# Performance work log

Hardware: AMD Instinct MI355X
Metric: run time of the kernel (lower is better)

The kernel has to match this reference:

```python
import jax, jax.numpy as jnp
import numpy as np

N = 8192          # total neurons (n)
IN_NEURONS = 1024 # input_neurons
OUT_NEURONS = 256 # output_neurons


def setup_inputs() -> dict:
    key = jax.random.key(0)
    k1, k2 = jax.random.split(key)
    x = jax.random.normal(k1, (1, IN_NEURONS), dtype=jnp.float32)
    # learned adjacency weight (original uses kaiming_uniform; scale kept small for stability)
    W = jax.random.normal(k2, (N, N), dtype=jnp.float32) * 0.01
    return {"x": x, "W": W, "num_steps": 4}


def reference(x, W, num_steps):
    n = W.shape[0]
    # load_input_neurons: state = (W.T * pad(x[0], n)).T  ==  W * s0[:, None]
    s0 = jnp.pad(x[0], (0, n - x.shape[1]))        # [n]
    state = W * s0[:, None]                        # [n, n]

    # step(): next = sum_i(W.T * state[i]) then .T  ==  W * colsum(state)[:, None]
    def body(state, _):
        col_sum = state.sum(axis=0)                # [n]
        return W * col_sum[:, None], None

    state, _ = jax.lax.scan(body, state, None, length=num_steps)

    # extract_output_neurons: diagonal entries state[-i, -i], i = OUT..1
    return jnp.diagonal(state)[-OUT_NEURONS:]      # [OUT_NEURONS]
```

## Files before the change

### kernel.cpp

```cpp
#include <hip/hip_runtime.h>


namespace {
constexpr int N = 8192;
constexpr int NF4 = N / 4;
constexpr int IN_N = 1024;
constexpr int OUT_N = 256;
constexpr int BT = 256;

constexpr int NCT = 8;
constexpr int R1R = 32;
constexpr int R2R = 128;
constexpr int SL1 = IN_N / R1R;
constexpr int SL2 = N / R2R;

constexpr size_t OFF_V1 = 0;
constexpr size_t OFF_V2 = 8192;
constexpr size_t OFF_V3 = 16384;
constexpr size_t OFF_V4 = 24576;
constexpr size_t OFF_P  = 32768;

typedef float f4 __attribute__((ext_vector_type(4)));
}

__global__ void zero_vecs(float* __restrict__ ws) {
  int i = blockIdx.x * blockDim.x + threadIdx.x;
  if (i < 3 * N + OUT_N) ws[i] = 0.0f;
}

template <int ROWS>
__global__ __launch_bounds__(BT) void gemv_slab(const float* __restrict__ W,
                                                const float* __restrict__ vin,
                                                float* __restrict__ P) {
  __shared__ float sv[ROWS];
  const int b = blockIdx.x, t = threadIdx.x;
  const int ct = b & (NCT - 1);
  const int rs = b >> 3;
  const int i0 = rs * ROWS;
  for (int i = t; i < ROWS; i += BT) sv[i] = vin[i0 + i];
  __syncthreads();
  const f4* __restrict__ W4 = reinterpret_cast<const f4*>(W);
  const int cf = ct * BT + t;
  f4 acc = (f4)(0.f);
#pragma unroll 8
  for (int i = 0; i < ROWS; ++i) {
    const f4 w = __builtin_nontemporal_load(W4 + (size_t)(i0 + i) * NF4 + cf);
    acc += w * sv[i];
  }
  reinterpret_cast<f4*>(P)[(size_t)rs * NF4 + cf] = acc;
}

template <int CS>
__global__ __launch_bounds__(BT) void reduce_cols(const float* __restrict__ P,
                                                  float* __restrict__ v) {
  const int j = blockIdx.x * BT + threadIdx.x;
  const int c0 = blockIdx.y * CS;
  float a = 0.f;
#pragma unroll
  for (int c = 0; c < CS; ++c) a += P[(size_t)(c0 + c) * N + j];
  atomicAdd(v + j, a);
}

__global__ __launch_bounds__(64) void gemv_tail(const float* __restrict__ W,
                                                const float* __restrict__ v3,
                                                float* __restrict__ v4) {
  __shared__ float sv[32];
  const int b = blockIdx.x, t = threadIdx.x;
  const int i0 = b * 32;
  if (t < 32) sv[t] = v3[i0 + t];
  __syncthreads();
  const f4* __restrict__ W4 = reinterpret_cast<const f4*>(W);
  f4 a = (f4)(0.f);
#pragma unroll 4
  for (int i = 0; i < 32; ++i) {
    const f4 w = W4[(size_t)(i0 + i) * NF4 + 1984 + t];
    a += w * sv[i];
  }
  atomicAdd(v4 + 4 * t + 0, a.x);
  atomicAdd(v4 + 4 * t + 1, a.y);
  atomicAdd(v4 + 4 * t + 2, a.z);
  atomicAdd(v4 + 4 * t + 3, a.w);
}

__global__ void diag_scale(const float* __restrict__ W,
                           const float* __restrict__ v4,
                           float* __restrict__ out) {
  const int t = threadIdx.x;
  const size_t j = (size_t)(N - OUT_N + t);
  out[t] = W[j * (N + 1)] * v4[t];
}

extern "C" void kernel_launch(void* const* d_in, const int* in_sizes, int n_in,
                              void* d_out, int out_size, void* d_ws, size_t ws_size,
                              hipStream_t stream) {
  const float* x = (const float*)d_in[0];
  const float* W = (const float*)d_in[1];
  float* ws = (float*)d_ws;
  float* v1 = ws + OFF_V1;
  float* v2 = ws + OFF_V2;
  float* v3 = ws + OFF_V3;
  float* v4 = ws + OFF_V4;
  float* P  = ws + OFF_P;
  float* out = (float*)d_out;

  zero_vecs<<<(3 * N + OUT_N + 255) / 256, 256, 0, stream>>>(ws);

  gemv_slab<R1R><<<SL1 * NCT, BT, 0, stream>>>(W, x, P);
  reduce_cols<16><<<dim3(N / BT, SL1 / 16), BT, 0, stream>>>(P, v1);

  gemv_slab<R2R><<<SL2 * NCT, BT, 0, stream>>>(W, v1, P);
  reduce_cols<16><<<dim3(N / BT, SL2 / 16), BT, 0, stream>>>(P, v2);

  gemv_slab<R2R><<<SL2 * NCT, BT, 0, stream>>>(W, v2, P);
  reduce_cols<16><<<dim3(N / BT, SL2 / 16), BT, 0, stream>>>(P, v3);

  gemv_tail<<<N / 32, 64, 0, stream>>>(W, v3, v4);

  diag_scale<<<1, OUT_N, 0, stream>>>(W, v4, out);
}
```

Measured before the change: 435.4 us.

## Fuse partial-sum reduction into GEMV via atomics and fold diagonal scale into tail

The GEMV slab kernels now accumulate their per-slab partial column sums straight into the output vector with float atomics, so the partial buffer P and the separate reduce_cols kernels go away. The tail kernel also multiplies by the diagonal entries and atomically adds into the output, which removes the diag_scale launch. The output is zeroed in the initial kernel, and the tail's W reads become nontemporal. This removes several launches and the P write/read round trip, in exchange for many more atomic operations (64 slabs per column) and nondeterministic summation order.

```diff
diff --git a/kernel.cpp b/kernel.cpp
--- a/kernel.cpp
+++ b/kernel.cpp
@@ -17,21 +17,20 @@
 constexpr size_t OFF_V1 = 0;
 constexpr size_t OFF_V2 = 8192;
 constexpr size_t OFF_V3 = 16384;
-constexpr size_t OFF_V4 = 24576;
-constexpr size_t OFF_P  = 32768;
 
 typedef float f4 __attribute__((ext_vector_type(4)));
 }
 
-__global__ void zero_vecs(float* __restrict__ ws) {
-  int i = blockIdx.x * blockDim.x + threadIdx.x;
-  if (i < 3 * N + OUT_N) ws[i] = 0.0f;
+__global__ void zero_vecs(float* __restrict__ ws, float* __restrict__ out) {
+  const int i = blockIdx.x * blockDim.x + threadIdx.x;
+  if (i < 3 * N) ws[i] = 0.0f;
+  if (i < OUT_N) out[i] = 0.0f;
 }
 
 template <int ROWS>
 __global__ __launch_bounds__(BT) void gemv_slab(const float* __restrict__ W,
                                                 const float* __restrict__ vin,
-                                                float* __restrict__ P) {
+                                                float* __restrict__ vout) {
   __shared__ float sv[ROWS];
   const int b = blockIdx.x, t = threadIdx.x;
   const int ct = b & (NCT - 1);
@@ -47,23 +46,16 @@
     const f4 w = __builtin_nontemporal_load(W4 + (size_t)(i0 + i) * NF4 + cf);
     acc += w * sv[i];
   }
-  reinterpret_cast<f4*>(P)[(size_t)rs * NF4 + cf] = acc;
-}
-
-template <int CS>
-__global__ __launch_bounds__(BT) void reduce_cols(const float* __restrict__ P,
-                                                  float* __restrict__ v) {
-  const int j = blockIdx.x * BT + threadIdx.x;
-  const int c0 = blockIdx.y * CS;
-  float a = 0.f;
-#pragma unroll
-  for (int c = 0; c < CS; ++c) a += P[(size_t)(c0 + c) * N + j];
-  atomicAdd(v + j, a);
+  float* __restrict__ o = vout + 4 * (size_t)cf;
+  atomicAdd(o + 0, acc.x);
+  atomicAdd(o + 1, acc.y);
+  atomicAdd(o + 2, acc.z);
+  atomicAdd(o + 3, acc.w);
 }
 
 __global__ __launch_bounds__(64) void gemv_tail(const float* __restrict__ W,
                                                 const float* __restrict__ v3,
-                                                float* __restrict__ v4) {
+                                                float* __restrict__ out) {
   __shared__ float sv[32];
   const int b = blockIdx.x, t = threadIdx.x;
   const int i0 = b * 32;
@@ -73,21 +65,18 @@
   f4 a = (f4)(0.f);
 #pragma unroll 4
   for (int i = 0; i < 32; ++i) {
-    const f4 w = W4[(size_t)(i0 + i) * NF4 + 1984 + t];
+    const f4 w = __builtin_nontemporal_load(W4 + (size_t)(i0 + i) * NF4 + 1984 + t);
     a += w * sv[i];
   }
-  atomicAdd(v4 + 4 * t + 0, a.x);
-  atomicAdd(v4 + 4 * t + 1, a.y);
-  atomicAdd(v4 + 4 * t + 2, a.z);
-  atomicAdd(v4 + 4 * t + 3, a.w);
-}
-
-__global__ void diag_scale(const float* __restrict__ W,
-                           const float* __restrict__ v4,
-                           float* __restrict__ out) {
-  const int t = threadIdx.x;
-  const size_t j = (size_t)(N - OUT_N + t);
-  out[t] = W[j * (N + 1)] * v4[t];
+  const int j0 = N - OUT_N + 4 * t;
+  const float d0 = W[(size_t)(j0 + 0) * N + (j0 + 0)];
+  const float d1 = W[(size_t)(j0 + 1) * N + (j0 + 1)];
+  const float d2 = W[(size_t)(j0 + 2) * N + (j0 + 2)];
+  const float d3 = W[(size_t)(j0 + 3) * N + (j0 + 3)];
+  atomicAdd(out + 4 * t + 0, d0 * a.x);
+  atomicAdd(out + 4 * t + 1, d1 * a.y);
+  atomicAdd(out + 4 * t + 2, d2 * a.z);
+  atomicAdd(out + 4 * t + 3, d3 * a.w);
 }
 
 extern "C" void kernel_launch(void* const* d_in, const int* in_sizes, int n_in,
@@ -99,22 +88,15 @@
   float* v1 = ws + OFF_V1;
   float* v2 = ws + OFF_V2;
   float* v3 = ws + OFF_V3;
-  float* v4 = ws + OFF_V4;
-  float* P  = ws + OFF_P;
   float* out = (float*)d_out;
 
-  zero_vecs<<<(3 * N + OUT_N + 255) / 256, 256, 0, stream>>>(ws);
+  zero_vecs<<<(3 * N + 255) / 256, 256, 0, stream>>>(ws, out);
 
-  gemv_slab<R1R><<<SL1 * NCT, BT, 0, stream>>>(W, x, P);
-  reduce_cols<16><<<dim3(N / BT, SL1 / 16), BT, 0, stream>>>(P, v1);
+  gemv_slab<R1R><<<SL1 * NCT, BT, 0, stream>>>(W, x, v1);
 
-  gemv_slab<R2R><<<SL2 * NCT, BT, 0, stream>>>(W, v1, P);
-  reduce_cols<16><<<dim3(N / BT, SL2 / 16), BT, 0, stream>>>(P, v2);
+  gemv_slab<R2R><<<SL2 * NCT, BT, 0, stream>>>(W, v1, v2);
 
-  gemv_slab<R2R><<<SL2 * NCT, BT, 0, stream>>>(W, v2, P);
-  reduce_cols<16><<<dim3(N / BT, SL2 / 16), BT, 0, stream>>>(P, v3);
+  gemv_slab<R2R><<<SL2 * NCT, BT, 0, stream>>>(W, v2, v3);
 
-  gemv_tail<<<N / 32, 64, 0, stream>>>(W, v3, v4);
-
-  diag_scale<<<1, OUT_N, 0, stream>>>(W, v4, out);
+  gemv_tail<<<N / 32, 64, 0, stream>>>(W, v3, out);
 }
```

Result: slower. 447.3 us (+2.7%).
